# Optimization experiments

Measured on AMD Instinct MI355X. Metric: run time of the kernel, lower is better.

Reference implementation:

```python
import jax, jax.numpy as jnp
import numpy as np

TAU_1 = 100.0


def setup_inputs() -> dict:
    key = jax.random.key(0)
    z = jax.random.normal(key, (8192, 512), dtype=jnp.float32)
    return {"z": z}


def reference(z) -> jnp.ndarray:
    # InfoNCE_l2 variant: log E_{i!=j}[ exp(-||z_i - z_j||^2 / tau_1) ]
    N = z.shape[0]
    sq = jnp.sum(z * z, axis=1)                      # [N]
    # squared euclidean distances: ||zi||^2 + ||zj||^2 - 2 zi.zj, clamped at 0
    D = jnp.maximum(sq[:, None] + sq[None, :] - 2.0 * (z @ z.T), 0.0)  # [N, N]
    E = jnp.exp(-D / TAU_1)
    # zero out the diagonal, average over the N*(N-1) off-diagonal entries
    off_diag_sum = jnp.sum(E) - jnp.sum(jnp.diagonal(E))
    mean_off = off_diag_sum / (N * (N - 1))
    return jnp.log(mean_off)
```

## Files before the change

kernel.cpp:

```cpp
#include <hip/hip_runtime.h>
#include <hip/hip_bf16.h>

#define NROWS 8192
#define KDIM  512
#define NT    64
#define NBLK  (NT*(NT+1)/2)
#define SCL1  0x7F7F7F7F
#define STRIP4 8192
#define C2    0.0144269504f

typedef __attribute__((ext_vector_type(16))) float f32x16;
typedef __attribute__((ext_vector_type(4))) int i32x4;
typedef __attribute__((ext_vector_type(8))) int i32x8;

__device__ __forceinline__ i32x8 mk_op4(i32x4 lo) {
    i32x8 r;
    r[0] = lo[0]; r[1] = lo[1]; r[2] = lo[2]; r[3] = lo[3];
    r[4] = 0; r[5] = 0; r[6] = 0; r[7] = 0;
    return r;
}

__device__ __forceinline__ int fp4_code(float x) {
    float v = fabsf(x);
    int c = v < 0.25f ? 0 : v < 0.75f ? 1 : v < 1.25f ? 2 : v < 1.75f ? 3
          : v < 2.5f  ? 4 : v < 3.5f  ? 5 : v < 5.0f  ? 6 : 7;
    return c | (x < 0.f ? 8 : 0);
}

__global__ __launch_bounds__(256) void prep_kernel(const float* __restrict__ z,
                                                   unsigned char* __restrict__ zb4,
                                                   float* __restrict__ nq) {
    int wave = threadIdx.x >> 6, lane = threadIdx.x & 63;
    int row = blockIdx.x * 4 + wave;
    const float* zr = z + (size_t)row * KDIM + lane * 8;
    float4 v0 = *(const float4*)zr;
    float4 v1 = *(const float4*)(zr + 4);
    float vals[8] = {v0.x, v0.y, v0.z, v0.w, v1.x, v1.y, v1.z, v1.w};
    float s = 0.f;
    unsigned int pk = 0u;
#pragma unroll
    for (int i = 0; i < 8; ++i) {
        s += vals[i] * vals[i];
        pk |= (unsigned int)fp4_code(vals[i]) << (4 * i);
    }
    int strip = row >> 5, lr = row & 31;
    size_t addr = (size_t)strip * STRIP4 + (lane >> 3) * 1024 +
                  ((lane >> 2) & 1) * 512 + lr * 16 + (lane & 3) * 4;
    *(unsigned int*)(zb4 + addr) = pk;
#pragma unroll
    for (int off = 32; off; off >>= 1) s += __shfl_down(s, off);
    if (lane == 0) nq[row] = -C2 * s;
}

__global__ __launch_bounds__(256, 3) void gram_kernel(const unsigned char* __restrict__ zb4,
                                                      const float* __restrict__ nq,
                                                      float* __restrict__ part) {
    __shared__ float wsum[4];

    int tid = threadIdx.x;
    int wave = tid >> 6, lane = tid & 63;
    int ln31 = lane & 31, kh = lane >> 5;
    int wm = wave >> 1, wn = wave & 1;

    int rem = blockIdx.x, bi = 0;
    while (rem >= NT - bi) { rem -= NT - bi; ++bi; }
    int bj = bi + rem;
    int rot = blockIdx.x & 7;

    int laneOff = kh * 512 + ln31 * 16;
    const unsigned char* pA0 = zb4 + (size_t)(bi * 4 + wm * 2) * STRIP4 + laneOff;
    const unsigned char* pA1 = pA0 + STRIP4;
    const unsigned char* pB0 = zb4 + (size_t)(bj * 4 + wn * 2) * STRIP4 + laneOff;
    const unsigned char* pB1 = pB0 + STRIP4;

    f32x16 accf[2][2];
#pragma unroll
    for (int mi = 0; mi < 2; ++mi)
#pragma unroll
        for (int ni = 0; ni < 2; ++ni)
#pragma unroll
            for (int r = 0; r < 16; ++r) accf[mi][ni][r] = 0.f;

#pragma unroll
    for (int ks = 0; ks < 8; ++ks) {
        int off = ((ks + rot) & 7) * 1024;
        i32x8 a0 = mk_op4(*(const i32x4*)(pA0 + off));
        i32x8 a1 = mk_op4(*(const i32x4*)(pA1 + off));
        i32x8 b0 = mk_op4(*(const i32x4*)(pB0 + off));
        i32x8 b1 = mk_op4(*(const i32x4*)(pB1 + off));
        accf[0][0] = __builtin_amdgcn_mfma_scale_f32_32x32x64_f8f6f4(a0, b0, accf[0][0], 4, 4, 0, SCL1, 0, SCL1);
        accf[0][1] = __builtin_amdgcn_mfma_scale_f32_32x32x64_f8f6f4(a0, b1, accf[0][1], 4, 4, 0, SCL1, 0, SCL1);
        accf[1][0] = __builtin_amdgcn_mfma_scale_f32_32x32x64_f8f6f4(a1, b0, accf[1][0], 4, 4, 0, SCL1, 0, SCL1);
        accf[1][1] = __builtin_amdgcn_mfma_scale_f32_32x32x64_f8f6f4(a1, b1, accf[1][1], 4, 4, 0, SCL1, 0, SCL1);
    }

    int rowBase = bi * 128 + wm * 64;
    int colBase = bj * 128 + wn * 64;
    float nqj[2] = { nq[colBase + ln31], nq[colBase + 32 + ln31] };

    float local = 0.f;
    if (bi != bj) {
#pragma unroll
        for (int mi = 0; mi < 2; ++mi) {
#pragma unroll
            for (int reg = 0; reg < 16; ++reg) {
                int rowf = (reg & 3) + 8 * (reg >> 2) + 4 * kh;
                float nqi = nq[rowBase + mi * 32 + rowf];
#pragma unroll
                for (int ni = 0; ni < 2; ++ni) {
                    float arg = fmaf(accf[mi][ni][reg], 2.f * C2, nqi + nqj[ni]);
                    local += __builtin_exp2f(fminf(arg, 0.f));
                }
            }
        }
    } else {
#pragma unroll
        for (int mi = 0; mi < 2; ++mi) {
#pragma unroll
            for (int reg = 0; reg < 16; ++reg) {
                int rowf = (reg & 3) + 8 * (reg >> 2) + 4 * kh;
                int gi = rowBase + mi * 32 + rowf;
                float nqi = nq[gi];
#pragma unroll
                for (int ni = 0; ni < 2; ++ni) {
                    int gj = colBase + ni * 32 + ln31;
                    float arg = fmaf(accf[mi][ni][reg], 2.f * C2, nqi + nqj[ni]);
                    float e = __builtin_exp2f(fminf(arg, 0.f));
                    local += (gi < gj) ? e : 0.f;
                }
            }
        }
    }

#pragma unroll
    for (int off = 32; off; off >>= 1) local += __shfl_down(local, off);
    if (lane == 0) wsum[wave] = local;
    __syncthreads();
    if (tid == 0) part[blockIdx.x] = wsum[0] + wsum[1] + wsum[2] + wsum[3];
}

__global__ __launch_bounds__(256) void reduce_kernel(const float* __restrict__ part,
                                                     float* __restrict__ out) {
    int tid = threadIdx.x;
    int wave = tid >> 6, lane = tid & 63;
    float s = 0.f;
    for (int i = tid; i < NBLK; i += 256) s += part[i];
#pragma unroll
    for (int off = 32; off; off >>= 1) s += __shfl_down(s, off);
    __shared__ float w[4];
    if (lane == 0) w[wave] = s;
    __syncthreads();
    if (tid == 0) {
        float total = 2.f * (w[0] + w[1] + w[2] + w[3]);
        out[0] = logf(total / ((float)NROWS * (float)(NROWS - 1)));
    }
}

extern "C" void kernel_launch(void* const* d_in, const int* in_sizes, int n_in,
                              void* d_out, int out_size, void* d_ws, size_t ws_size,
                              hipStream_t stream) {
    const float* z = (const float*)d_in[0];
    float* out = (float*)d_out;
    unsigned char* zb4 = (unsigned char*)d_ws;
    float* nq = (float*)((char*)d_ws + (size_t)NROWS * KDIM / 2);
    float* part = nq + NROWS;

    prep_kernel<<<NROWS / 4, 256, 0, stream>>>(z, zb4, nq);
    gram_kernel<<<NBLK, 256, 0, stream>>>(zb4, nq, part);
    reduce_kernel<<<1, 256, 0, stream>>>(part, out);
}
```

Before: 85.80 us.

## Stage tiles via global_load_lds and fuse final reduction with atomic last-block

Loads each block's A and B fp4 strips into 64KB of LDS using async global-to-LDS copies, so waves read their operands from shared memory instead of repeatedly from global. Occupancy is lowered to 2 blocks per CU to fit the LDS. The separate reduce kernel is removed: each block publishes its partial and increments an atomic counter, and the last block computes the final log. This saves a launch but adds an atomic and a barrier that serializes load and compute.

```diff
diff --git a/kernel.cpp b/kernel.cpp
--- a/kernel.cpp
+++ b/kernel.cpp
@@ -1,5 +1,4 @@
 #include <hip/hip_runtime.h>
-#include <hip/hip_bf16.h>
 
 #define NROWS 8192
 #define KDIM  512
@@ -13,6 +12,10 @@
 typedef __attribute__((ext_vector_type(4))) int i32x4;
 typedef __attribute__((ext_vector_type(8))) int i32x8;
 
+#define GLDS(g, l) __builtin_amdgcn_global_load_lds( \
+    (const __attribute__((address_space(1))) void*)(g), \
+    (__attribute__((address_space(3))) void*)(l), 16, 0, 0)
+
 __device__ __forceinline__ i32x8 mk_op4(i32x4 lo) {
     i32x8 r;
     r[0] = lo[0]; r[1] = lo[1]; r[2] = lo[2]; r[3] = lo[3];
@@ -29,7 +32,9 @@
 
 __global__ __launch_bounds__(256) void prep_kernel(const float* __restrict__ z,
                                                    unsigned char* __restrict__ zb4,
-                                                   float* __restrict__ nq) {
+                                                   float* __restrict__ nq,
+                                                   int* __restrict__ cnt) {
+    if (blockIdx.x == 0 && threadIdx.x == 0) *cnt = 0;
     int wave = threadIdx.x >> 6, lane = threadIdx.x & 63;
     int row = blockIdx.x * 4 + wave;
     const float* zr = z + (size_t)row * KDIM + lane * 8;
@@ -52,10 +57,14 @@
     if (lane == 0) nq[row] = -C2 * s;
 }
 
-__global__ __launch_bounds__(256, 3) void gram_kernel(const unsigned char* __restrict__ zb4,
+__global__ __launch_bounds__(256, 2) void gram_kernel(const unsigned char* __restrict__ zb4,
                                                       const float* __restrict__ nq,
-                                                      float* __restrict__ part) {
+                                                      float* __restrict__ part,
+                                                      int* __restrict__ cnt,
+                                                      float* __restrict__ out) {
+    __shared__ unsigned char lds[65536];
     __shared__ float wsum[4];
+    __shared__ int lastFlag;
 
     int tid = threadIdx.x;
     int wave = tid >> 6, lane = tid & 63;
@@ -67,10 +76,23 @@
     int bj = bi + rem;
     int rot = blockIdx.x & 7;
 
+    const unsigned char* srcA = zb4 + (size_t)(bi * 4) * STRIP4;
+    const unsigned char* srcB = zb4 + (size_t)(bj * 4) * STRIP4;
+    {
+        int lo = tid * 16;
+        int wbase = wave * 1024;
+#pragma unroll
+        for (int i = 0; i < 8; ++i)
+            GLDS(srcA + i * 4096 + lo, lds + i * 4096 + wbase);
+#pragma unroll
+        for (int i = 0; i < 8; ++i)
+            GLDS(srcB + i * 4096 + lo, lds + 32768 + i * 4096 + wbase);
+    }
+
     int laneOff = kh * 512 + ln31 * 16;
-    const unsigned char* pA0 = zb4 + (size_t)(bi * 4 + wm * 2) * STRIP4 + laneOff;
+    const unsigned char* pA0 = lds + (wm * 2) * STRIP4 + laneOff;
     const unsigned char* pA1 = pA0 + STRIP4;
-    const unsigned char* pB0 = zb4 + (size_t)(bj * 4 + wn * 2) * STRIP4 + laneOff;
+    const unsigned char* pB0 = lds + 32768 + (wn * 2) * STRIP4 + laneOff;
     const unsigned char* pB1 = pB0 + STRIP4;
 
     f32x16 accf[2][2];
@@ -80,6 +102,8 @@
         for (int ni = 0; ni < 2; ++ni)
 #pragma unroll
             for (int r = 0; r < 16; ++r) accf[mi][ni][r] = 0.f;
+
+    __syncthreads();
 
 #pragma unroll
     for (int ks = 0; ks < 8; ++ks) {
@@ -136,23 +160,30 @@
     for (int off = 32; off; off >>= 1) local += __shfl_down(local, off);
     if (lane == 0) wsum[wave] = local;
     __syncthreads();
-    if (tid == 0) part[blockIdx.x] = wsum[0] + wsum[1] + wsum[2] + wsum[3];
-}
-
-__global__ __launch_bounds__(256) void reduce_kernel(const float* __restrict__ part,
-                                                     float* __restrict__ out) {
-    int tid = threadIdx.x;
-    int wave = tid >> 6, lane = tid & 63;
-    float s = 0.f;
-    for (int i = tid; i < NBLK; i += 256) s += part[i];
-#pragma unroll
-    for (int off = 32; off; off >>= 1) s += __shfl_down(s, off);
-    __shared__ float w[4];
-    if (lane == 0) w[wave] = s;
+
+    if (tid == 0) {
+        float val = wsum[0] + wsum[1] + wsum[2] + wsum[3];
+        __hip_atomic_store(&part[blockIdx.x], val, __ATOMIC_RELEASE,
+                           __HIP_MEMORY_SCOPE_AGENT);
+        int old = __hip_atomic_fetch_add(cnt, 1, __ATOMIC_ACQ_REL,
+                                         __HIP_MEMORY_SCOPE_AGENT);
+        lastFlag = (old == NBLK - 1);
+    }
     __syncthreads();
-    if (tid == 0) {
-        float total = 2.f * (w[0] + w[1] + w[2] + w[3]);
-        out[0] = logf(total / ((float)NROWS * (float)(NROWS - 1)));
+
+    if (lastFlag) {
+        float s = 0.f;
+        for (int i = tid; i < NBLK; i += 256)
+            s += __hip_atomic_load(&part[i], __ATOMIC_RELAXED,
+                                   __HIP_MEMORY_SCOPE_AGENT);
+#pragma unroll
+        for (int off = 32; off; off >>= 1) s += __shfl_down(s, off);
+        if (lane == 0) wsum[wave] = s;
+        __syncthreads();
+        if (tid == 0) {
+            float total = 2.f * (wsum[0] + wsum[1] + wsum[2] + wsum[3]);
+            out[0] = logf(total / ((float)NROWS * (float)(NROWS - 1)));
+        }
     }
 }
 
@@ -164,8 +195,8 @@
     unsigned char* zb4 = (unsigned char*)d_ws;
     float* nq = (float*)((char*)d_ws + (size_t)NROWS * KDIM / 2);
     float* part = nq + NROWS;
-
-    prep_kernel<<<NROWS / 4, 256, 0, stream>>>(z, zb4, nq);
-    gram_kernel<<<NBLK, 256, 0, stream>>>(zb4, nq, part);
-    reduce_kernel<<<1, 256, 0, stream>>>(part, out);
-}
+    int* cnt = (int*)(part + NBLK);
+
+    prep_kernel<<<NROWS / 4, 256, 0, stream>>>(z, zb4, nq, cnt);
+    gram_kernel<<<NBLK, 256, 0, stream>>>(zb4, nq, part, cnt, out);
+}
```

After: 125.7 us. 46.5% more time.

## Use 128x256 block tiles over the upper triangle with wider per-wave N

Applied to the files above, without the earlier changes.

Each block now covers 128 rows by 256 columns, and every wave computes a 64x128 sub-tile with 8 accumulators instead of 4. This halves the number of column block-tiles and reuses each A fragment across four B fragments, cutting global/L2 operand traffic per MFMA. Block indices are mapped to (bi,bj) pairs with a closed-form sqrt plus correction, replacing the old linear search. Register pressure rises and occupancy drops to 2 waves per SIMD. Blocks on the diagonal now compute some tiles that fall entirely below it, and the mask skips that work.

```diff
diff --git a/kernel.cpp b/kernel.cpp
--- a/kernel.cpp
+++ b/kernel.cpp
@@ -1,10 +1,9 @@
 #include <hip/hip_runtime.h>
-#include <hip/hip_bf16.h>
 
 #define NROWS 8192
 #define KDIM  512
-#define NT    64
-#define NBLK  (NT*(NT+1)/2)
+#define NTJ   32
+#define NBLK  1056
 #define SCL1  0x7F7F7F7F
 #define STRIP4 8192
 #define C2    0.0144269504f
@@ -52,7 +51,7 @@
     if (lane == 0) nq[row] = -C2 * s;
 }
 
-__global__ __launch_bounds__(256, 3) void gram_kernel(const unsigned char* __restrict__ zb4,
+__global__ __launch_bounds__(256, 2) void gram_kernel(const unsigned char* __restrict__ zb4,
                                                       const float* __restrict__ nq,
                                                       float* __restrict__ part) {
     __shared__ float wsum[4];
@@ -62,44 +61,52 @@
     int ln31 = lane & 31, kh = lane >> 5;
     int wm = wave >> 1, wn = wave & 1;
 
-    int rem = blockIdx.x, bi = 0;
-    while (rem >= NT - bi) { rem -= NT - bi; ++bi; }
-    int bj = bi + rem;
+    int x = blockIdx.x;
+    int bj = (int)((__builtin_sqrtf(4.0f * (float)x + 1.0f) - 1.0f) * 0.5f);
+    while ((bj + 1) * (bj + 2) <= x) ++bj;
+    while (bj * (bj + 1) > x) --bj;
+    int bi = x - bj * (bj + 1);
     int rot = blockIdx.x & 7;
 
     int laneOff = kh * 512 + ln31 * 16;
     const unsigned char* pA0 = zb4 + (size_t)(bi * 4 + wm * 2) * STRIP4 + laneOff;
     const unsigned char* pA1 = pA0 + STRIP4;
-    const unsigned char* pB0 = zb4 + (size_t)(bj * 4 + wn * 2) * STRIP4 + laneOff;
-    const unsigned char* pB1 = pB0 + STRIP4;
+    const unsigned char* pB  = zb4 + (size_t)(bj * 8 + wn * 4) * STRIP4 + laneOff;
 
-    f32x16 accf[2][2];
+    f32x16 accf[2][4];
 #pragma unroll
     for (int mi = 0; mi < 2; ++mi)
 #pragma unroll
-        for (int ni = 0; ni < 2; ++ni)
+        for (int nj = 0; nj < 4; ++nj)
 #pragma unroll
-            for (int r = 0; r < 16; ++r) accf[mi][ni][r] = 0.f;
+            for (int r = 0; r < 16; ++r) accf[mi][nj][r] = 0.f;
 
 #pragma unroll
     for (int ks = 0; ks < 8; ++ks) {
         int off = ((ks + rot) & 7) * 1024;
         i32x8 a0 = mk_op4(*(const i32x4*)(pA0 + off));
         i32x8 a1 = mk_op4(*(const i32x4*)(pA1 + off));
-        i32x8 b0 = mk_op4(*(const i32x4*)(pB0 + off));
-        i32x8 b1 = mk_op4(*(const i32x4*)(pB1 + off));
+        i32x8 b0 = mk_op4(*(const i32x4*)(pB + off));
+        i32x8 b1 = mk_op4(*(const i32x4*)(pB + STRIP4 + off));
+        i32x8 b2 = mk_op4(*(const i32x4*)(pB + 2 * STRIP4 + off));
+        i32x8 b3 = mk_op4(*(const i32x4*)(pB + 3 * STRIP4 + off));
         accf[0][0] = __builtin_amdgcn_mfma_scale_f32_32x32x64_f8f6f4(a0, b0, accf[0][0], 4, 4, 0, SCL1, 0, SCL1);
         accf[0][1] = __builtin_amdgcn_mfma_scale_f32_32x32x64_f8f6f4(a0, b1, accf[0][1], 4, 4, 0, SCL1, 0, SCL1);
+        accf[0][2] = __builtin_amdgcn_mfma_scale_f32_32x32x64_f8f6f4(a0, b2, accf[0][2], 4, 4, 0, SCL1, 0, SCL1);
+        accf[0][3] = __builtin_amdgcn_mfma_scale_f32_32x32x64_f8f6f4(a0, b3, accf[0][3], 4, 4, 0, SCL1, 0, SCL1);
         accf[1][0] = __builtin_amdgcn_mfma_scale_f32_32x32x64_f8f6f4(a1, b0, accf[1][0], 4, 4, 0, SCL1, 0, SCL1);
         accf[1][1] = __builtin_amdgcn_mfma_scale_f32_32x32x64_f8f6f4(a1, b1, accf[1][1], 4, 4, 0, SCL1, 0, SCL1);
+        accf[1][2] = __builtin_amdgcn_mfma_scale_f32_32x32x64_f8f6f4(a1, b2, accf[1][2], 4, 4, 0, SCL1, 0, SCL1);
+        accf[1][3] = __builtin_amdgcn_mfma_scale_f32_32x32x64_f8f6f4(a1, b3, accf[1][3], 4, 4, 0, SCL1, 0, SCL1);
     }
 
     int rowBase = bi * 128 + wm * 64;
-    int colBase = bj * 128 + wn * 64;
-    float nqj[2] = { nq[colBase + ln31], nq[colBase + 32 + ln31] };
+    int colBase = bj * 256 + wn * 128;
+    float local = 0.f;
 
-    float local = 0.f;
-    if (bi != bj) {
+    if (rowBase + 64 <= colBase) {
+        float nqj[4] = { nq[colBase + ln31],      nq[colBase + 32 + ln31],
+                         nq[colBase + 64 + ln31], nq[colBase + 96 + ln31] };
 #pragma unroll
         for (int mi = 0; mi < 2; ++mi) {
 #pragma unroll
@@ -107,13 +114,15 @@
                 int rowf = (reg & 3) + 8 * (reg >> 2) + 4 * kh;
                 float nqi = nq[rowBase + mi * 32 + rowf];
 #pragma unroll
-                for (int ni = 0; ni < 2; ++ni) {
-                    float arg = fmaf(accf[mi][ni][reg], 2.f * C2, nqi + nqj[ni]);
+                for (int nj = 0; nj < 4; ++nj) {
+                    float arg = fmaf(accf[mi][nj][reg], 2.f * C2, nqi + nqj[nj]);
                     local += __builtin_exp2f(fminf(arg, 0.f));
                 }
             }
         }
-    } else {
+    } else if (rowBase <= colBase + 127) {
+        float nqj[4] = { nq[colBase + ln31],      nq[colBase + 32 + ln31],
+                         nq[colBase + 64 + ln31], nq[colBase + 96 + ln31] };
 #pragma unroll
         for (int mi = 0; mi < 2; ++mi) {
 #pragma unroll
@@ -122,9 +131,9 @@
                 int gi = rowBase + mi * 32 + rowf;
                 float nqi = nq[gi];
 #pragma unroll
-                for (int ni = 0; ni < 2; ++ni) {
-                    int gj = colBase + ni * 32 + ln31;
-                    float arg = fmaf(accf[mi][ni][reg], 2.f * C2, nqi + nqj[ni]);
+                for (int nj = 0; nj < 4; ++nj) {
+                    int gj = colBase + nj * 32 + ln31;
+                    float arg = fmaf(accf[mi][nj][reg], 2.f * C2, nqi + nqj[nj]);
                     float e = __builtin_exp2f(fminf(arg, 0.f));
                     local += (gi < gj) ? e : 0.f;
                 }
```

After: 86.22 us. About the same (+0.5%).
